# Kernel optimization log

Hardware: AMD Instinct MI355X
Metric: run time of the kernel (lower is better)

The kernel has to match this reference:

```python
import jax, jax.numpy as jnp
import numpy as np

ALPHA = (0.02, 0.04, 0.08, 0.16)
CHAMFER_W, SMOOTH_W, CURVATURE_W = 1.0, 1.0, 0.3
NS = (8192, 4096, 2048, 1024)
B = 2


def _sqdist(a, b):
    # a: [B,N,3], b: [B,M,3] -> [B,N,M] squared euclidean distance
    return (jnp.sum(a * a, axis=-1)[:, :, None]
            - 2.0 * jnp.einsum('bnc,bmc->bnm', a, b)
            + jnp.sum(b * b, axis=-1)[:, None, :])


def _knn(d, k):
    # k smallest distances + indices along last axis
    neg, idx = jax.lax.top_k(-d, k)
    return -neg, idx


def _gather(points, idx):
    # points: [B,M,C], idx: [B,N,K] -> [B,N,K,C]
    return jax.vmap(lambda p, i: p[i])(points, idx)


def _scale_loss(pc1, pc2, flow):
    # pc1, pc2, flow: [B,3,N]-like -> permute to points-last layout
    p1 = jnp.transpose(pc1, (0, 2, 1))   # [B,N,3]
    p2 = jnp.transpose(pc2, (0, 2, 1))   # [B,M,3]
    fl = jnp.transpose(flow, (0, 2, 1))  # [B,N,3]
    warp = p1 + fl                        # warped pc1

    # curvature of pc2 (10-NN on pc2 itself)
    _, k22 = _knn(_sqdist(p2, p2), 10)
    cv2 = jnp.sum(_gather(p2, k22) - p2[:, :, None, :], axis=2) / 9.0  # [B,M,3]

    # 10-NN on pc1 (shared for warped curvature and smoothness; 9-NN is prefix)
    _, k11 = _knn(_sqdist(p1, p1), 10)
    cvw = jnp.sum(_gather(warp, k11) - warp[:, :, None, :], axis=2) / 9.0  # [B,N,3]

    k9 = k11[:, :, :9]
    gfl = _gather(fl, k9)  # [B,N,9,3]
    smooth = jnp.sum(jnp.linalg.norm(gfl - fl[:, :, None, :], axis=3), axis=2) / 8.0  # [B,N]

    # chamfer between warped pc1 and pc2
    d12 = _sqdist(warp, p2)               # [B,N,M]
    dist1 = jnp.min(d12, axis=-1)         # [B,N]
    dist2 = jnp.min(d12, axis=1)          # [B,M]

    # inverse-distance interpolation of pc2 curvature onto warped pc1 (5-NN)
    dist, kidx = _knn(d12, 5)             # [B,N,5]
    gcv = _gather(cv2, kidx)              # [B,N,5,3]
    w = 1.0 / (dist + 1e-8)
    w = w / jnp.sum(w, axis=2, keepdims=True)
    inter = jnp.sum(w[..., None] * gcv, axis=2)  # [B,N,3]

    chamfer = jnp.mean(jnp.sum(dist1, axis=1)) + jnp.mean(jnp.sum(dist2, axis=1))
    smoothness = jnp.mean(jnp.sum(smooth, axis=1))
    curv = jnp.mean(jnp.sum(jnp.sum((inter - cvw) ** 2, axis=2), axis=1))
    return chamfer, smoothness, curv


def setup_inputs() -> dict:
    key = jax.random.key(0)
    keys = jax.random.split(key, 12)
    out = {}
    names = ['pc1', 'pc2', 'flow']
    k = 0
    for name in names:
        for i, n in enumerate(NS):
            scale = 1.0 if name != 'flow' else 0.1
            out[f'{name}_{i}'] = scale * jax.random.normal(keys[k], (B, 3, n), dtype=jnp.float32)
            k += 1
    return out


def reference(pc1_0, pc1_1, pc1_2, pc1_3,
              pc2_0, pc2_1, pc2_2, pc2_3,
              flow_0, flow_1, flow_2, flow_3):
    pcs1 = (pc1_0, pc1_1, pc1_2, pc1_3)
    pcs2 = (pc2_0, pc2_1, pc2_2, pc2_3)
    flows = (flow_0, flow_1, flow_2, flow_3)
    ch = sm = cv = jnp.float32(0.0)
    for a, p1, p2, fl in zip(ALPHA, pcs1, pcs2, flows):
        c, s, k = _scale_loss(p1, p2, fl)
        ch = ch + a * c
        sm = sm + a * s
        cv = cv + a * k
    total = CHAMFER_W * ch + CURVATURE_W * cv + SMOOTH_W * sm
    return jnp.reshape(total, (1,))
```

## Files before the change

### kernel.cpp

```cpp
#include <hip/hip_runtime.h>
#include <math.h>


#define BLOCK 512
#define UNIT 1024
#define NTOT 15360
#define MASKC 0xFFFFE000u
#define PB 340

typedef unsigned int uint;

struct Params {
  const float* pc1[4];
  const float* pc2[4];
  const float* fl[4];
  float4* cv2;
  float4* cvw;
  float* out;
};

__device__ __forceinline__ void decode(int r, int wv, int& s, int& b,
                                       int& i0, int& lo, int& N, int& cpw,
                                       int& off, float& alpha) {
  int rr;
  if (r < 256)      { s = 0; rr = r; }
  else if (r < 320) { s = 1; rr = r - 256; }
  else if (r < 336) { s = 2; rr = r - 320; }
  else              { s = 3; rr = r - 336; }
  N = 8192 >> s;
  cpw = 8 >> s;
  int perb = 128 >> (2 * s);
  b = rr >> (7 - 2 * s);
  int chunk = rr & (perb - 1);
  int qg = (chunk << s) + (wv >> (3 - s));
  i0 = qg << 6;
  lo = (wv & (cpw - 1)) << 10;
  off = 16384 - (16384 >> s);
  alpha = 0.02f * (float)(1 << s);
}

__device__ __forceinline__ float wave_sum(float v) {
  #pragma unroll
  for (int o = 32; o; o >>= 1) v += __shfl_down(v, o, 64);
  return v;
}

template <int K>
__device__ __forceinline__ void key_insert(float (&kd)[K], float kf) {
  #pragma unroll
  for (int m = K - 1; m >= 1; --m)
    kd[m] = __builtin_amdgcn_fmed3f(kf, kd[m - 1], kd[m]);
  kd[0] = fminf(kd[0], kf);
}

template <int K>
__device__ __forceinline__ void merge_pair(float (&a)[K], const float (&b)[K]) {
  #pragma unroll
  for (int m = 0; m < K; ++m) key_insert<K>(a, b[m]);
}

__device__ __forceinline__ float pack_key(float d, float iw) {
  return __uint_as_float((__float_as_uint(d) & MASKC) | __float_as_uint(iw));
}

template <int K, bool WARP, bool PACK>
__device__ void scan_u(const float* px, const float* py, const float* pz,
                       const float* fx, const float* fy, const float* fz,
                       int lo, float ax, float ay, float az,
                       float (&a)[K], float (&b)[K], float4* tile,
                       int lane) {
  int j = lo + lane;
  float x = px[j], y = py[j], z = pz[j];
  if (WARP) { x += fx[j]; y += fy[j]; z += fz[j]; }
  for (int c0 = lo; c0 < lo + UNIT; c0 += 64) {
    tile[lane] = make_float4(x, y, z, __uint_as_float((uint)(c0 + lane)));
    asm volatile("s_waitcnt lgkmcnt(0)" ::: "memory");
    if (c0 + 64 < lo + UNIT) {
      int jn = j + 64;
      x = px[jn]; y = py[jn]; z = pz[jn];
      if (WARP) { x += fx[jn]; y += fy[jn]; z += fz[jn]; }
    }
    #pragma unroll 8
    for (int t = 0; t < 64; t += 2) {
      float4 cA = tile[t];
      float4 cB = tile[t + 1];
      float dxa = ax - cA.x, dya = ay - cA.y, dza = az - cA.z;
      float dA = fmaf(dxa, dxa, fmaf(dya, dya, dza * dza));
      float dxb = ax - cB.x, dyb = ay - cB.y, dzb = az - cB.z;
      float dB = fmaf(dxb, dxb, fmaf(dyb, dyb, dzb * dzb));
      if (PACK) {
        key_insert<K>(a, pack_key(dA, cA.w));
        key_insert<K>(b, pack_key(dB, cB.w));
      } else {
        a[0] = fminf(a[0], dA);
        b[0] = fminf(b[0], dB);
      }
    }
    j += 64;
  }
}

template <int K>
__device__ __forceinline__ bool merge_group(float (&a)[K], float* sm,
                                            int tid, int cpw) {
  const int STR = K | 1;
  int q = tid & 63, wv = tid >> 6;
  #pragma unroll
  for (int m = 0; m < K; ++m) sm[(wv * 64 + q) * STR + m] = a[m];
  __syncthreads();
  if (wv & (cpw - 1)) return false;
  for (int w = wv + 1; w < wv + cpw; ++w)
    #pragma unroll
    for (int m = 0; m < K; ++m)
      key_insert<K>(a, sm[(w * 64 + q) * STR + m]);
  return true;
}

__global__ __launch_bounds__(1) void k_zero(float* out) { out[0] = 0.f; }

__global__ __launch_bounds__(BLOCK, 8) void k_fused(Params P) {
  __shared__ float4 tiles[8][64];
  __shared__ float sm[8 * 64 * 11];
  int tid = threadIdx.x, q = tid & 63, wv = tid >> 6;
  int pass = blockIdx.x / PB, r = blockIdx.x % PB;
  int s, b, i0, lo, N, cpw, off; float alpha;
  decode(r, wv, s, b, i0, lo, N, cpw, off, alpha);
  int i = i0 + q;
  float4* tile = tiles[wv];

  if (pass == 0) {
    const float* p2 = P.pc2[s] + b * 3 * N;
    float ax = p2[i], ay = p2[N + i], az = p2[2 * N + i];
    float a[10], bb[10];
    #pragma unroll
    for (int m = 0; m < 10; ++m) { a[m] = 3.0e38f; bb[m] = 3.0e38f; }
    scan_u<10, false, true>(p2, p2 + N, p2 + 2 * N, nullptr, nullptr,
                            nullptr, lo, ax, ay, az, a, bb, tile, q);
    merge_pair<10>(a, bb);
    if (!merge_group<10>(a, sm, tid, cpw)) return;
    float sx = 0.f, sy = 0.f, sz = 0.f;
    #pragma unroll
    for (int m = 0; m < 10; ++m) {
      int j = (int)(__float_as_uint(a[m]) & 0x1FFFu);
      sx += p2[j]; sy += p2[N + j]; sz += p2[2 * N + j];
    }
    const float inv9 = 1.f / 9.f;
    P.cv2[b * NTOT + off + i] = make_float4((sx - 10.f * ax) * inv9,
                                            (sy - 10.f * ay) * inv9,
                                            (sz - 10.f * az) * inv9, 0.f);
  } else if (pass == 1) {
    const float* p1 = P.pc1[s] + b * 3 * N;
    const float* fl = P.fl[s] + b * 3 * N;
    float ax = p1[i], ay = p1[N + i], az = p1[2 * N + i];
    float a[10], bb[10];
    #pragma unroll
    for (int m = 0; m < 10; ++m) { a[m] = 3.0e38f; bb[m] = 3.0e38f; }
    scan_u<10, false, true>(p1, p1 + N, p1 + 2 * N, nullptr, nullptr,
                            nullptr, lo, ax, ay, az, a, bb, tile, q);
    merge_pair<10>(a, bb);
    if (!merge_group<10>(a, sm, tid, cpw)) return;
    float fix = fl[i], fiy = fl[N + i], fiz = fl[2 * N + i];
    float wix = ax + fix, wiy = ay + fiy, wiz = az + fiz;
    float sx = 0.f, sy = 0.f, sz = 0.f, smooth = 0.f;
    float dmax = -1.f, worst = 0.f;
    #pragma unroll
    for (int m = 0; m < 10; ++m) {
      int j = (int)(__float_as_uint(a[m]) & 0x1FFFu);
      float px = p1[j], py = p1[N + j], pz = p1[2 * N + j];
      float flx = fl[j], fly = fl[N + j], flz = fl[2 * N + j];
      sx += px + flx; sy += py + fly; sz += pz + flz;
      float ddx = px - ax, ddy = py - ay, ddz = pz - az;
      float d = fmaf(ddx, ddx, fmaf(ddy, ddy, ddz * ddz));
      float gx = flx - fix, gy = fly - fiy, gz = flz - fiz;
      float term = sqrtf(fmaf(gx, gx, fmaf(gy, gy, gz * gz)));
      smooth += term;
      if (d > dmax) { dmax = d; worst = term; }
    }
    smooth -= worst;
    const float inv9 = 1.f / 9.f;
    P.cvw[b * NTOT + off + i] = make_float4((sx - 10.f * wix) * inv9,
                                            (sy - 10.f * wiy) * inv9,
                                            (sz - 10.f * wiz) * inv9, 0.f);
    float ssum = wave_sum(smooth * (1.f / 8.f));
    if (q == 0) atomicAdd(P.out, alpha * 0.5f * ssum);
  } else {
    const float* p1 = P.pc1[s] + b * 3 * N;
    const float* fl = P.fl[s] + b * 3 * N;
    const float* p2 = P.pc2[s] + b * 3 * N;
    float ax = p2[i], ay = p2[N + i], az = p2[2 * N + i];
    float a[1], bb[1];
    a[0] = 3.0e38f; bb[0] = 3.0e38f;
    scan_u<1, true, false>(p1, p1 + N, p1 + 2 * N, fl, fl + N, fl + 2 * N,
                           lo, ax, ay, az, a, bb, tile, q);
    merge_pair<1>(a, bb);
    if (!merge_group<1>(a, sm, tid, cpw)) return;
    float msum = wave_sum(a[0]);
    if (q == 0) atomicAdd(P.out, alpha * 0.5f * msum);
  }
}

__global__ __launch_bounds__(BLOCK, 8) void k_cross(Params P) {
  __shared__ float4 tiles[8][64];
  __shared__ float sm[8 * 64 * 5];
  int tid = threadIdx.x, q = tid & 63, wv = tid >> 6;
  int s, b, i0, lo, N, cpw, off; float alpha;
  decode(blockIdx.x, wv, s, b, i0, lo, N, cpw, off, alpha);
  int i = i0 + q;
  const float* p1 = P.pc1[s] + b * 3 * N;
  const float* fl = P.fl[s] + b * 3 * N;
  const float* p2 = P.pc2[s] + b * 3 * N;
  float ax = p1[i] + fl[i], ay = p1[N + i] + fl[N + i],
        az = p1[2 * N + i] + fl[2 * N + i];
  float a[5], bb[5];
  #pragma unroll
  for (int m = 0; m < 5; ++m) { a[m] = 3.0e38f; bb[m] = 3.0e38f; }
  scan_u<5, false, true>(p2, p2 + N, p2 + 2 * N, nullptr, nullptr, nullptr,
                         lo, ax, ay, az, a, bb, tiles[wv], q);
  merge_pair<5>(a, bb);
  if (!merge_group<5>(a, sm, tid, cpw)) return;
  float dist1 = 3.0e38f, wsum = 0.f, ix = 0.f, iy = 0.f, iz = 0.f;
  #pragma unroll
  for (int m = 0; m < 5; ++m) {
    int j = (int)(__float_as_uint(a[m]) & 0x1FFFu);
    float px = p2[j], py = p2[N + j], pz = p2[2 * N + j];
    float ddx = px - ax, ddy = py - ay, ddz = pz - az;
    float d = fmaf(ddx, ddx, fmaf(ddy, ddy, ddz * ddz));
    dist1 = fminf(dist1, d);
    float w = 1.f / (d + 1e-8f);
    wsum += w;
    float4 cv = P.cv2[b * NTOT + off + j];
    ix += w * cv.x; iy += w * cv.y; iz += w * cv.z;
  }
  float inv = 1.f / wsum;
  ix *= inv; iy *= inv; iz *= inv;
  float4 cw = P.cvw[b * NTOT + off + i];
  float ex = ix - cw.x, ey = iy - cw.y, ez = iz - cw.z;
  float curv = fmaf(ex, ex, fmaf(ey, ey, ez * ez));
  float csum = wave_sum(dist1 + 0.3f * curv);
  if (q == 0) atomicAdd(P.out, alpha * 0.5f * csum);
}

extern "C" void kernel_launch(void* const* d_in, const int* in_sizes, int n_in,
                              void* d_out, int out_size, void* d_ws,
                              size_t ws_size, hipStream_t stream) {
  Params P;
  for (int s = 0; s < 4; ++s) {
    P.pc1[s] = (const float*)d_in[s];
    P.pc2[s] = (const float*)d_in[4 + s];
    P.fl[s]  = (const float*)d_in[8 + s];
  }
  P.cv2 = (float4*)d_ws;
  P.cvw = (float4*)((char*)d_ws + (size_t)2 * NTOT * sizeof(float4));
  P.out = (float*)d_out;

  k_zero<<<dim3(1), dim3(1), 0, stream>>>(P.out);
  k_fused<<<dim3(3 * PB), dim3(BLOCK), 0, stream>>>(P);
  k_cross<<<dim3(PB), dim3(BLOCK), 0, stream>>>(P);
}
```

Baseline: 326.5 us.

## Fold cross kNN scan into fused kernel and split off epilogue kernel

Moves the warped-pc1 to pc2 5-NN scan into the main fused kernel as a fourth pass, so it runs concurrently with the self-kNN and chamfer passes. The found neighbour keys are written to workspace. A new lightweight per-point epilogue kernel then computes dist1 and the curvature interpolation using cv2/cvw. This removes the serialization between the big kernel and the cross scan, at the cost of extra global traffic for the keys and one more launch.

```diff
diff --git a/kernel.cpp b/kernel.cpp
--- a/kernel.cpp
+++ b/kernel.cpp
@@ -16,6 +16,7 @@
   const float* fl[4];
   float4* cv2;
   float4* cvw;
+  float* keys;
   float* out;
 };
 
@@ -183,7 +184,7 @@
                                             (sz - 10.f * wiz) * inv9, 0.f);
     float ssum = wave_sum(smooth * (1.f / 8.f));
     if (q == 0) atomicAdd(P.out, alpha * 0.5f * ssum);
-  } else {
+  } else if (pass == 2) {
     const float* p1 = P.pc1[s] + b * 3 * N;
     const float* fl = P.fl[s] + b * 3 * N;
     const float* p2 = P.pc2[s] + b * 3 * N;
@@ -196,32 +197,47 @@
     if (!merge_group<1>(a, sm, tid, cpw)) return;
     float msum = wave_sum(a[0]);
     if (q == 0) atomicAdd(P.out, alpha * 0.5f * msum);
-  }
-}
-
-__global__ __launch_bounds__(BLOCK, 8) void k_cross(Params P) {
-  __shared__ float4 tiles[8][64];
-  __shared__ float sm[8 * 64 * 5];
-  int tid = threadIdx.x, q = tid & 63, wv = tid >> 6;
-  int s, b, i0, lo, N, cpw, off; float alpha;
-  decode(blockIdx.x, wv, s, b, i0, lo, N, cpw, off, alpha);
-  int i = i0 + q;
+  } else {
+    const float* p1 = P.pc1[s] + b * 3 * N;
+    const float* fl = P.fl[s] + b * 3 * N;
+    const float* p2 = P.pc2[s] + b * 3 * N;
+    float ax = p1[i] + fl[i], ay = p1[N + i] + fl[N + i],
+          az = p1[2 * N + i] + fl[2 * N + i];
+    float a[5], bb[5];
+    #pragma unroll
+    for (int m = 0; m < 5; ++m) { a[m] = 3.0e38f; bb[m] = 3.0e38f; }
+    scan_u<5, false, true>(p2, p2 + N, p2 + 2 * N, nullptr, nullptr,
+                           nullptr, lo, ax, ay, az, a, bb, tile, q);
+    merge_pair<5>(a, bb);
+    if (!merge_group<5>(a, sm, tid, cpw)) return;
+    #pragma unroll
+    for (int m = 0; m < 5; ++m)
+      P.keys[m * (2 * NTOT) + b * NTOT + off + i] = a[m];
+  }
+}
+
+__global__ __launch_bounds__(256) void k_epi(Params P) {
+  int t = blockIdx.x * 256 + threadIdx.x;
+  int b = t >= NTOT;
+  int r = t - b * NTOT;
+  int s, i;
+  if (r < 8192)       { s = 0; i = r; }
+  else if (r < 12288) { s = 1; i = r - 8192; }
+  else if (r < 14336) { s = 2; i = r - 12288; }
+  else                { s = 3; i = r - 14336; }
+  int N = 8192 >> s;
+  int off = 16384 - (16384 >> s);
+  float alpha = 0.02f * (float)(1 << s);
   const float* p1 = P.pc1[s] + b * 3 * N;
   const float* fl = P.fl[s] + b * 3 * N;
   const float* p2 = P.pc2[s] + b * 3 * N;
   float ax = p1[i] + fl[i], ay = p1[N + i] + fl[N + i],
         az = p1[2 * N + i] + fl[2 * N + i];
-  float a[5], bb[5];
-  #pragma unroll
-  for (int m = 0; m < 5; ++m) { a[m] = 3.0e38f; bb[m] = 3.0e38f; }
-  scan_u<5, false, true>(p2, p2 + N, p2 + 2 * N, nullptr, nullptr, nullptr,
-                         lo, ax, ay, az, a, bb, tiles[wv], q);
-  merge_pair<5>(a, bb);
-  if (!merge_group<5>(a, sm, tid, cpw)) return;
   float dist1 = 3.0e38f, wsum = 0.f, ix = 0.f, iy = 0.f, iz = 0.f;
   #pragma unroll
   for (int m = 0; m < 5; ++m) {
-    int j = (int)(__float_as_uint(a[m]) & 0x1FFFu);
+    uint key = __float_as_uint(P.keys[m * (2 * NTOT) + b * NTOT + off + i]);
+    int j = (int)(key & 0x1FFFu);
     float px = p2[j], py = p2[N + j], pz = p2[2 * N + j];
     float ddx = px - ax, ddy = py - ay, ddz = pz - az;
     float d = fmaf(ddx, ddx, fmaf(ddy, ddy, ddz * ddz));
@@ -236,8 +252,9 @@
   float4 cw = P.cvw[b * NTOT + off + i];
   float ex = ix - cw.x, ey = iy - cw.y, ez = iz - cw.z;
   float curv = fmaf(ex, ex, fmaf(ey, ey, ez * ez));
-  float csum = wave_sum(dist1 + 0.3f * curv);
-  if (q == 0) atomicAdd(P.out, alpha * 0.5f * csum);
+  float v = alpha * 0.5f * (dist1 + 0.3f * curv);
+  v = wave_sum(v);
+  if ((threadIdx.x & 63) == 0) atomicAdd(P.out, v);
 }
 
 extern "C" void kernel_launch(void* const* d_in, const int* in_sizes, int n_in,
@@ -251,9 +268,10 @@
   }
   P.cv2 = (float4*)d_ws;
   P.cvw = (float4*)((char*)d_ws + (size_t)2 * NTOT * sizeof(float4));
+  P.keys = (float*)((char*)d_ws + (size_t)4 * NTOT * sizeof(float4));
   P.out = (float*)d_out;
 
   k_zero<<<dim3(1), dim3(1), 0, stream>>>(P.out);
-  k_fused<<<dim3(3 * PB), dim3(BLOCK), 0, stream>>>(P);
-  k_cross<<<dim3(PB), dim3(BLOCK), 0, stream>>>(P);
-}
+  k_fused<<<dim3(4 * PB), dim3(BLOCK), 0, stream>>>(P);
+  k_epi<<<dim3((2 * NTOT) / 256), dim3(256), 0, stream>>>(P);
+}
```

New measurement: 309.0 us. 1.06x faster.
